# Performance work log

Measured on AMD Instinct MI355X. Metric: run time of the kernel, lower is better.

Reference implementation:

```python
import jax, jax.numpy as jnp
import numpy as np

HEADS = 8
DIM_HEAD = 64
DIM = 512
SCALE = DIM ** -0.5  # NOTE: original scales by dim**-0.5, not dim_head**-0.5


def setup_inputs() -> dict:
    key = jax.random.key(0)
    k1, k2, k3 = jax.random.split(key, 3)
    b, n = 2, 4096
    x = jax.random.normal(k1, (b, n, DIM), dtype=jnp.float32)
    Wqkv = jax.random.normal(k2, (DIM, 3 * HEADS * DIM_HEAD), dtype=jnp.float32) * (DIM ** -0.5)
    Wout = jax.random.normal(k3, (HEADS * DIM_HEAD, DIM), dtype=jnp.float32) * ((HEADS * DIM_HEAD) ** -0.5)
    b_out = jnp.zeros((DIM,), dtype=jnp.float32)
    return {"x": x, "Wqkv": Wqkv, "Wout": Wout, "b_out": b_out}


def reference(x, Wqkv, Wout, b_out):
    b, n, _ = x.shape
    h, d = HEADS, DIM_HEAD
    qkv = x @ Wqkv  # [b, n, 3*h*d]
    q, k, v = jnp.split(qkv, 3, axis=-1)
    to_heads = lambda t: t.reshape(b, n, h, d).transpose(0, 2, 1, 3)  # [b,h,n,d]
    q, k, v = to_heads(q), to_heads(k), to_heads(v)
    half = n // 2
    q_s, q_t = q[:, :, :half], q[:, :, half:]
    k_t = k[:, :, half:]  # k_s is unused in the original module
    v_s, v_t = v[:, :, :half], v[:, :, half:]
    # temporal branch: q_t attends to k_t, reads v_t
    dots_t = jnp.einsum('bhid,bhjd->bhij', q_t, k_t) * SCALE
    # spatial branch: cross-term q_s attends to k_t, reads v_s
    dots_s = jnp.einsum('bhid,bhjd->bhij', q_s, k_t) * SCALE
    attn_s = jax.nn.softmax(dots_s, axis=-1)
    attn_t = jax.nn.softmax(dots_t, axis=-1)
    out_s = jnp.einsum('bhij,bhjd->bhid', attn_s, v_s)
    out_t = jnp.einsum('bhij,bhjd->bhid', attn_t, v_t)
    out = jnp.concatenate([out_s, out_t], axis=2)  # [b,h,n,d]
    out = out.transpose(0, 2, 1, 3).reshape(b, n, h * d)
    return out @ Wout + b_out
```

## Files before the change

### kernel.cpp

```cpp
#include <hip/hip_runtime.h>
#include <hip/hip_bf16.h>

typedef __bf16 bf16;
typedef _Float16 f16;
typedef __bf16 bf16x4 __attribute__((ext_vector_type(4)));
typedef __bf16 bf16x8 __attribute__((ext_vector_type(8)));
typedef _Float16 f16x4 __attribute__((ext_vector_type(4)));
typedef _Float16 f16x8 __attribute__((ext_vector_type(8)));
typedef float floatx4 __attribute__((ext_vector_type(4)));

static __device__ __forceinline__ floatx4 mfma_bf16(bf16x8 a, bf16x8 b, floatx4 c) {
  return __builtin_amdgcn_mfma_f32_16x16x32_bf16(a, b, c, 0, 0, 0);
}
static __device__ __forceinline__ floatx4 mfma_f16k16(f16x4 a, f16x4 b, floatx4 c) {
  return __builtin_amdgcn_mfma_f32_16x16x16f16(a, b, c, 0, 0, 0);
}

static __device__ __forceinline__ bf16x8 ldcvt8(const float* __restrict__ src) {
  float4 f0 = *reinterpret_cast<const float4*>(src);
  float4 f1 = *reinterpret_cast<const float4*>(src + 4);
  bf16x8 r;
  r[0] = (bf16)f0.x; r[1] = (bf16)f0.y; r[2] = (bf16)f0.z; r[3] = (bf16)f0.w;
  r[4] = (bf16)f1.x; r[5] = (bf16)f1.y; r[6] = (bf16)f1.z; r[7] = (bf16)f1.w;
  return r;
}

#define HEADS 8
#define DIMH 64
#define DIM 512
#define SEQ 4096
#define HALF 2048
#define BATCH 2
#define MROWS (BATCH * SEQ)
#define ELEMS ((size_t)MROWS * DIM)

#define C2F (0.044194173824159216f * 1.4426950408889634f)

__global__ __launch_bounds__(256)
void transpose_cvt(const float* __restrict__ src, bf16* __restrict__ dst,
                   int K, int N) {
  __shared__ float tile[32][33];
  const int n0 = blockIdx.x * 32, k0 = blockIdx.y * 32;
  const int t = threadIdx.x;
  const int r = t >> 3, c4 = (t & 7) * 4;
  float4 v = *reinterpret_cast<const float4*>(src + (size_t)(k0 + r) * N + n0 + c4);
  tile[r][c4 + 0] = v.x; tile[r][c4 + 1] = v.y;
  tile[r][c4 + 2] = v.z; tile[r][c4 + 3] = v.w;
  __syncthreads();
  bf16x4 o;
#pragma unroll
  for (int i = 0; i < 4; ++i) o[i] = (bf16)tile[c4 + i][r];
  *reinterpret_cast<bf16x4*>(dst + (size_t)(n0 + r) * K + k0 + c4) = o;
}

__global__ __launch_bounds__(256)
void qkv_gemm(const float* __restrict__ X, const bf16* __restrict__ Wt,
              bf16* __restrict__ Qw, bf16* __restrict__ Kw, f16* __restrict__ Vt) {
  constexpr int Kd = DIM;
  __shared__ __align__(16) bf16 smem[5120];
  bf16 (*As)[40] = (bf16(*)[40])smem;
  bf16 (*Bs)[40] = (bf16(*)[40])(smem + 2560);
  f16 (*Ts)[72] = (f16(*)[72])smem;

  const int m0 = blockIdx.x * 64, n0 = blockIdx.y * 64;
  const int t = threadIdx.x;
  const int wave = t >> 6, lane = t & 63, quad = lane >> 4, l16 = lane & 15;
  const int m_off = (wave >> 1) * 32, n_off = (wave & 1) * 32;

  floatx4 acc[2][2] = {};
  const int srow = t >> 2, scol = (t & 3) * 8;

  for (int k0 = 0; k0 < Kd; k0 += 32) {
    bf16x8 av = ldcvt8(X + (size_t)(m0 + srow) * Kd + k0 + scol);
    bf16x8 bv = *reinterpret_cast<const bf16x8*>(Wt + (size_t)(n0 + srow) * Kd + k0 + scol);
    *reinterpret_cast<bf16x8*>(&As[srow][scol]) = av;
    *reinterpret_cast<bf16x8*>(&Bs[srow][scol]) = bv;
    __syncthreads();

    bf16x8 a0 = *reinterpret_cast<const bf16x8*>(&As[m_off + l16][quad * 8]);
    bf16x8 a1 = *reinterpret_cast<const bf16x8*>(&As[m_off + 16 + l16][quad * 8]);
    bf16x8 b0 = *reinterpret_cast<const bf16x8*>(&Bs[n_off + l16][quad * 8]);
    bf16x8 b1 = *reinterpret_cast<const bf16x8*>(&Bs[n_off + 16 + l16][quad * 8]);
    acc[0][0] = mfma_bf16(a0, b0, acc[0][0]);
    acc[0][1] = mfma_bf16(a0, b1, acc[0][1]);
    acc[1][0] = mfma_bf16(a1, b0, acc[1][0]);
    acc[1][1] = mfma_bf16(a1, b1, acc[1][1]);
    __syncthreads();
  }

  if (n0 < 1024) {
#pragma unroll
    for (int mi = 0; mi < 2; ++mi)
#pragma unroll
      for (int ni = 0; ni < 2; ++ni)
#pragma unroll
        for (int r = 0; r < 4; ++r) {
          int row = m0 + m_off + mi * 16 + quad * 4 + r;
          int col = n0 + n_off + ni * 16 + l16;
          int which = col >> 9, cc = col & 511;
          int head = cc >> 6, dim = cc & 63;
          int bb = row >> 12, nn = row & 4095;
          float val = acc[mi][ni][r];
          if (which == 0) val *= C2F;
          bf16* dst = which ? Kw : Qw;
          dst[(((size_t)(bb * HEADS + head)) * SEQ + nn) * DIMH + dim] = (bf16)val;
        }
  } else {
    int head = (n0 - 1024) >> 6;
#pragma unroll
    for (int mi = 0; mi < 2; ++mi)
#pragma unroll
      for (int ni = 0; ni < 2; ++ni)
#pragma unroll
        for (int r = 0; r < 4; ++r)
          Ts[n_off + ni * 16 + l16][m_off + mi * 16 + quad * 4 + r] = (f16)acc[mi][ni][r];
    __syncthreads();
    int bb = m0 >> 12, nnb = m0 & 4095;
    size_t base = ((size_t)(bb * HEADS + head)) * DIMH;
#pragma unroll
    for (int it = 0; it < 2; ++it) {
      int idx = t + it * 256;
      int dim = idx >> 3, ns = (idx & 7) * 8;
      *reinterpret_cast<f16x8*>(Vt + (base + dim) * SEQ + nnb + ns) =
          *reinterpret_cast<const f16x8*>(&Ts[dim][ns]);
    }
  }
}

__global__ __launch_bounds__(256)
void attn_kernel(const bf16* __restrict__ Q, const bf16* __restrict__ K,
                 const f16* __restrict__ Vt, bf16* __restrict__ Ow) {
  const int qt = blockIdx.x, h = blockIdx.y, bb = blockIdx.z;
  const int t = threadIdx.x;
  const int wave = t >> 6, lane = t & 63, quad = lane >> 4, l16 = lane & 15;

  __shared__ bf16 Ks[64][72];
  __shared__ f16 VsT[64][72];

  const size_t hb = ((size_t)(bb * HEADS + h)) * SEQ * DIMH;
  const int vbase = (qt < 16) ? 0 : HALF;
  const int q0 = qt * 128 + wave * 32;

  bf16x8 qa[2][2];
#pragma unroll
  for (int mt = 0; mt < 2; ++mt)
#pragma unroll
    for (int kc = 0; kc < 2; ++kc)
      qa[mt][kc] = *reinterpret_cast<const bf16x8*>(
          Q + hb + (size_t)(q0 + mt * 16 + l16) * DIMH + kc * 32 + quad * 8);

  floatx4 o_acc[2][4] = {};
  float l_acc[2] = {0.f, 0.f};

  for (int kc0 = 0; kc0 < HALF; kc0 += 64) {
    __syncthreads();
#pragma unroll
    for (int it = 0; it < 2; ++it) {
      int idx = t + it * 256;
      int row = idx >> 3, g = idx & 7;
      bf16x8 kv = *reinterpret_cast<const bf16x8*>(
          K + hb + (size_t)(HALF + kc0 + row) * DIMH + g * 8);
      *reinterpret_cast<bf16x8*>(&Ks[row][g * 8]) = kv;
      f16x8 vv = *reinterpret_cast<const f16x8*>(
          Vt + hb + (size_t)row * SEQ + vbase + kc0 + g * 8);
      *reinterpret_cast<f16x8*>(&VsT[row][g * 8]) = vv;
    }
    __syncthreads();

#pragma unroll
    for (int kt = 0; kt < 4; ++kt) {
      bf16x8 ka0 = *reinterpret_cast<const bf16x8*>(&Ks[kt * 16 + l16][quad * 8]);
      bf16x8 ka1 = *reinterpret_cast<const bf16x8*>(&Ks[kt * 16 + l16][32 + quad * 8]);

      f16x4 pb[2];
#pragma unroll
      for (int mt = 0; mt < 2; ++mt) {
        floatx4 st = {0.f, 0.f, 0.f, 0.f};
        st = mfma_bf16(ka0, qa[mt][0], st);
        st = mfma_bf16(ka1, qa[mt][1], st);
        float lsum = l_acc[mt];
#pragma unroll
        for (int r = 0; r < 4; ++r) {
          float p = __builtin_amdgcn_exp2f(st[r]);
          lsum += p;
          pb[mt][r] = (f16)p;
        }
        l_acc[mt] = lsum;
      }

#pragma unroll
      for (int dsub = 0; dsub < 4; ++dsub) {
        f16x4 va = *reinterpret_cast<const f16x4*>(
            &VsT[dsub * 16 + l16][kt * 16 + quad * 4]);
        o_acc[0][dsub] = mfma_f16k16(va, pb[0], o_acc[0][dsub]);
        o_acc[1][dsub] = mfma_f16k16(va, pb[1], o_acc[1][dsub]);
      }
    }
  }

  float inv[2];
#pragma unroll
  for (int mt = 0; mt < 2; ++mt) {
    float v = l_acc[mt];
    v += __shfl_xor(v, 16);
    v += __shfl_xor(v, 32);
    inv[mt] = 1.0f / v;
  }

#pragma unroll
  for (int mt = 0; mt < 2; ++mt) {
    int n = q0 + mt * 16 + l16;
    size_t rowbase = ((size_t)(bb * SEQ + n)) * DIM + h * DIMH;
#pragma unroll
    for (int dsub = 0; dsub < 4; ++dsub) {
      bf16x4 ov;
#pragma unroll
      for (int r = 0; r < 4; ++r) ov[r] = (bf16)(o_acc[mt][dsub][r] * inv[mt]);
      *reinterpret_cast<bf16x4*>(Ow + rowbase + dsub * 16 + quad * 4) = ov;
    }
  }
}

__global__ __launch_bounds__(256)
void out_gemm(const bf16* __restrict__ A, const bf16* __restrict__ Wt,
              const float* __restrict__ bias, float* __restrict__ out) {
  constexpr int Kd = DIM;
  __shared__ bf16 As[64][40];
  __shared__ bf16 Bs[64][40];

  const int m0 = blockIdx.x * 64, n0 = blockIdx.y * 64;
  const int t = threadIdx.x;
  const int wave = t >> 6, lane = t & 63, quad = lane >> 4, l16 = lane & 15;
  const int m_off = (wave >> 1) * 32, n_off = (wave & 1) * 32;

  floatx4 acc[2][2] = {};
  const int srow = t >> 2, scol = (t & 3) * 8;

  for (int k0 = 0; k0 < Kd; k0 += 32) {
    bf16x8 av = *reinterpret_cast<const bf16x8*>(A + (size_t)(m0 + srow) * Kd + k0 + scol);
    bf16x8 bv = *reinterpret_cast<const bf16x8*>(Wt + (size_t)(n0 + srow) * Kd + k0 + scol);
    *reinterpret_cast<bf16x8*>(&As[srow][scol]) = av;
    *reinterpret_cast<bf16x8*>(&Bs[srow][scol]) = bv;
    __syncthreads();

    bf16x8 a0 = *reinterpret_cast<const bf16x8*>(&As[m_off + l16][quad * 8]);
    bf16x8 a1 = *reinterpret_cast<const bf16x8*>(&As[m_off + 16 + l16][quad * 8]);
    bf16x8 b0 = *reinterpret_cast<const bf16x8*>(&Bs[n_off + l16][quad * 8]);
    bf16x8 b1 = *reinterpret_cast<const bf16x8*>(&Bs[n_off + 16 + l16][quad * 8]);
    acc[0][0] = mfma_bf16(a0, b0, acc[0][0]);
    acc[0][1] = mfma_bf16(a0, b1, acc[0][1]);
    acc[1][0] = mfma_bf16(a1, b0, acc[1][0]);
    acc[1][1] = mfma_bf16(a1, b1, acc[1][1]);
    __syncthreads();
  }

#pragma unroll
  for (int mi = 0; mi < 2; ++mi)
#pragma unroll
    for (int ni = 0; ni < 2; ++ni)
#pragma unroll
      for (int r = 0; r < 4; ++r) {
        int row = m0 + m_off + mi * 16 + quad * 4 + r;
        int col = n0 + n_off + ni * 16 + l16;
        out[(size_t)row * DIM + col] = acc[mi][ni][r] + bias[col];
      }
}

extern "C" void kernel_launch(void* const* d_in, const int* in_sizes, int n_in,
                              void* d_out, int out_size, void* d_ws, size_t ws_size,
                              hipStream_t stream) {
  const float* x = (const float*)d_in[0];
  const float* wqkv = (const float*)d_in[1];
  const float* wout = (const float*)d_in[2];
  const float* bout = (const float*)d_in[3];
  float* out = (float*)d_out;

  bf16* Qw = (bf16*)d_ws;
  bf16* Kw = Qw + ELEMS;
  f16* Vt = (f16*)(Kw + ELEMS);
  bf16* Ow = (bf16*)(Vt + ELEMS);
  bf16* WtQKV = Ow + ELEMS;
  bf16* WtOUT = WtQKV + (size_t)1536 * 512;

  transpose_cvt<<<dim3(1536 / 32, DIM / 32), 256, 0, stream>>>(wqkv, WtQKV, DIM, 1536);
  transpose_cvt<<<dim3(DIM / 32, DIM / 32), 256, 0, stream>>>(wout, WtOUT, DIM, DIM);
  qkv_gemm<<<dim3(MROWS / 64, 1536 / 64), 256, 0, stream>>>(x, WtQKV, Qw, Kw, Vt);
  attn_kernel<<<dim3(SEQ / 128, HEADS, BATCH), 256, 0, stream>>>(Qw, Kw, Vt, Ow);
  out_gemm<<<dim3(MROWS / 64, DIM / 64), 256, 0, stream>>>(Ow, WtOUT, bout, out);
}
```

Baseline: 194.2 us.

## Retile QKV GEMM to 128x128, prefetch tiles in registers, shrink attention tiles

The QKV GEMM moves to 128x128 block tiles with 64x64 per wave and a register-prefetched next K slice, so each staged tile is reused more. The attention kernel handles 16 query rows per wave, 64 per block, which doubles the grid and adds register prefetch of K/V chunks plus an occupancy hint. The output GEMM also prefetches its next K slice into registers. The trade-off is more K/V reloads in attention and higher register pressure in the GEMM.

```diff
diff --git a/kernel.cpp b/kernel.cpp
--- a/kernel.cpp
+++ b/kernel.cpp
@@ -16,9 +16,7 @@
   return __builtin_amdgcn_mfma_f32_16x16x16f16(a, b, c, 0, 0, 0);
 }
 
-static __device__ __forceinline__ bf16x8 ldcvt8(const float* __restrict__ src) {
-  float4 f0 = *reinterpret_cast<const float4*>(src);
-  float4 f1 = *reinterpret_cast<const float4*>(src + 4);
+static __device__ __forceinline__ bf16x8 cvt8(float4 f0, float4 f1) {
   bf16x8 r;
   r[0] = (bf16)f0.x; r[1] = (bf16)f0.y; r[2] = (bf16)f0.z; r[3] = (bf16)f0.w;
   r[4] = (bf16)f1.x; r[5] = (bf16)f1.y; r[6] = (bf16)f1.z; r[7] = (bf16)f1.w;
@@ -56,47 +54,68 @@
 __global__ __launch_bounds__(256)
 void qkv_gemm(const float* __restrict__ X, const bf16* __restrict__ Wt,
               bf16* __restrict__ Qw, bf16* __restrict__ Kw, f16* __restrict__ Vt) {
-  constexpr int Kd = DIM;
-  __shared__ __align__(16) bf16 smem[5120];
-  bf16 (*As)[40] = (bf16(*)[40])smem;
-  bf16 (*Bs)[40] = (bf16(*)[40])(smem + 2560);
-  f16 (*Ts)[72] = (f16(*)[72])smem;
-
-  const int m0 = blockIdx.x * 64, n0 = blockIdx.y * 64;
+  __shared__ __align__(16) char smem_raw[36864];
+  bf16 (*As)[40] = (bf16(*)[40])smem_raw;
+  bf16 (*Bs)[40] = (bf16(*)[40])(smem_raw + 10240);
+
+  const int m0 = blockIdx.x * 128, n0 = blockIdx.y * 128;
   const int t = threadIdx.x;
   const int wave = t >> 6, lane = t & 63, quad = lane >> 4, l16 = lane & 15;
-  const int m_off = (wave >> 1) * 32, n_off = (wave & 1) * 32;
-
-  floatx4 acc[2][2] = {};
-  const int srow = t >> 2, scol = (t & 3) * 8;
-
-  for (int k0 = 0; k0 < Kd; k0 += 32) {
-    bf16x8 av = ldcvt8(X + (size_t)(m0 + srow) * Kd + k0 + scol);
-    bf16x8 bv = *reinterpret_cast<const bf16x8*>(Wt + (size_t)(n0 + srow) * Kd + k0 + scol);
-    *reinterpret_cast<bf16x8*>(&As[srow][scol]) = av;
-    *reinterpret_cast<bf16x8*>(&Bs[srow][scol]) = bv;
-    __syncthreads();
-
-    bf16x8 a0 = *reinterpret_cast<const bf16x8*>(&As[m_off + l16][quad * 8]);
-    bf16x8 a1 = *reinterpret_cast<const bf16x8*>(&As[m_off + 16 + l16][quad * 8]);
-    bf16x8 b0 = *reinterpret_cast<const bf16x8*>(&Bs[n_off + l16][quad * 8]);
-    bf16x8 b1 = *reinterpret_cast<const bf16x8*>(&Bs[n_off + 16 + l16][quad * 8]);
-    acc[0][0] = mfma_bf16(a0, b0, acc[0][0]);
-    acc[0][1] = mfma_bf16(a0, b1, acc[0][1]);
-    acc[1][0] = mfma_bf16(a1, b0, acc[1][0]);
-    acc[1][1] = mfma_bf16(a1, b1, acc[1][1]);
-    __syncthreads();
+  const int wr = wave >> 1, wc = wave & 1;
+
+  f16 (*Ts)[72] = (f16(*)[72])(smem_raw + wave * 9216);
+
+  floatx4 acc[4][4] = {};
+
+  float4 a0r[2], a1r[2];
+  bf16x8 breg[2];
+  auto loadk = [&](int k0) {
+#pragma unroll
+    for (int it = 0; it < 2; ++it) {
+      int idx = t + it * 256, row = idx >> 2, c8 = (idx & 3) * 8;
+      const float* xp = X + (size_t)(m0 + row) * DIM + k0 + c8;
+      a0r[it] = *reinterpret_cast<const float4*>(xp);
+      a1r[it] = *reinterpret_cast<const float4*>(xp + 4);
+      breg[it] = *reinterpret_cast<const bf16x8*>(Wt + (size_t)(n0 + row) * DIM + k0 + c8);
+    }
+  };
+
+  loadk(0);
+  for (int k0 = 0; k0 < DIM; k0 += 32) {
+    __syncthreads();
+#pragma unroll
+    for (int it = 0; it < 2; ++it) {
+      int idx = t + it * 256, row = idx >> 2, c8 = (idx & 3) * 8;
+      *reinterpret_cast<bf16x8*>(&As[row][c8]) = cvt8(a0r[it], a1r[it]);
+      *reinterpret_cast<bf16x8*>(&Bs[row][c8]) = breg[it];
+    }
+    __syncthreads();
+    int nk = k0 + 32; if (nk >= DIM) nk = 0;
+    loadk(nk);
+
+    bf16x8 af[4], bfr[4];
+#pragma unroll
+    for (int mi = 0; mi < 4; ++mi)
+      af[mi] = *reinterpret_cast<const bf16x8*>(&As[wr * 64 + mi * 16 + l16][quad * 8]);
+#pragma unroll
+    for (int ni = 0; ni < 4; ++ni)
+      bfr[ni] = *reinterpret_cast<const bf16x8*>(&Bs[wc * 64 + ni * 16 + l16][quad * 8]);
+#pragma unroll
+    for (int mi = 0; mi < 4; ++mi)
+#pragma unroll
+      for (int ni = 0; ni < 4; ++ni)
+        acc[mi][ni] = mfma_bf16(af[mi], bfr[ni], acc[mi][ni]);
   }
 
   if (n0 < 1024) {
 #pragma unroll
-    for (int mi = 0; mi < 2; ++mi)
-#pragma unroll
-      for (int ni = 0; ni < 2; ++ni)
+    for (int mi = 0; mi < 4; ++mi)
+#pragma unroll
+      for (int ni = 0; ni < 4; ++ni)
 #pragma unroll
         for (int r = 0; r < 4; ++r) {
-          int row = m0 + m_off + mi * 16 + quad * 4 + r;
-          int col = n0 + n_off + ni * 16 + l16;
+          int row = m0 + wr * 64 + mi * 16 + quad * 4 + r;
+          int col = n0 + wc * 64 + ni * 16 + l16;
           int which = col >> 9, cc = col & 511;
           int head = cc >> 6, dim = cc & 63;
           int bb = row >> 12, nn = row & 4095;
@@ -106,118 +125,115 @@
           dst[(((size_t)(bb * HEADS + head)) * SEQ + nn) * DIMH + dim] = (bf16)val;
         }
   } else {
-    int head = (n0 - 1024) >> 6;
-#pragma unroll
-    for (int mi = 0; mi < 2; ++mi)
-#pragma unroll
-      for (int ni = 0; ni < 2; ++ni)
-#pragma unroll
-        for (int r = 0; r < 4; ++r)
-          Ts[n_off + ni * 16 + l16][m_off + mi * 16 + quad * 4 + r] = (f16)acc[mi][ni][r];
-    __syncthreads();
-    int bb = m0 >> 12, nnb = m0 & 4095;
+    __syncthreads();
+    int head = (n0 + wc * 64 - 1024) >> 6;
+#pragma unroll
+    for (int mi = 0; mi < 4; ++mi)
+#pragma unroll
+      for (int ni = 0; ni < 4; ++ni) {
+        f16x4 pv;
+#pragma unroll
+        for (int r = 0; r < 4; ++r) pv[r] = (f16)acc[mi][ni][r];
+        *reinterpret_cast<f16x4*>(&Ts[ni * 16 + l16][mi * 16 + quad * 4]) = pv;
+      }
+    int bb = m0 >> 12, nnb = (m0 + wr * 64) & 4095;
     size_t base = ((size_t)(bb * HEADS + head)) * DIMH;
 #pragma unroll
-    for (int it = 0; it < 2; ++it) {
-      int idx = t + it * 256;
-      int dim = idx >> 3, ns = (idx & 7) * 8;
-      *reinterpret_cast<f16x8*>(Vt + (base + dim) * SEQ + nnb + ns) =
-          *reinterpret_cast<const f16x8*>(&Ts[dim][ns]);
-    }
-  }
-}
-
-__global__ __launch_bounds__(256)
+    for (int it = 0; it < 8; ++it) {
+      int idx = lane + it * 64;
+      int d = idx >> 3, ns = (idx & 7) * 8;
+      *reinterpret_cast<f16x8*>(Vt + (base + d) * SEQ + nnb + ns) =
+          *reinterpret_cast<const f16x8*>(&Ts[d][ns]);
+    }
+  }
+}
+
+__global__ __launch_bounds__(256, 4)
 void attn_kernel(const bf16* __restrict__ Q, const bf16* __restrict__ K,
                  const f16* __restrict__ Vt, bf16* __restrict__ Ow) {
   const int qt = blockIdx.x, h = blockIdx.y, bb = blockIdx.z;
   const int t = threadIdx.x;
-  const int wave = t >> 6, lane = t & 63, quad = lane >> 4, l16 = lane & 15;
+  const int lane = t & 63, quad = lane >> 4, l16 = lane & 15;
+  const int wave = t >> 6;
 
   __shared__ bf16 Ks[64][72];
   __shared__ f16 VsT[64][72];
 
   const size_t hb = ((size_t)(bb * HEADS + h)) * SEQ * DIMH;
-  const int vbase = (qt < 16) ? 0 : HALF;
-  const int q0 = qt * 128 + wave * 32;
-
-  bf16x8 qa[2][2];
-#pragma unroll
-  for (int mt = 0; mt < 2; ++mt)
-#pragma unroll
-    for (int kc = 0; kc < 2; ++kc)
-      qa[mt][kc] = *reinterpret_cast<const bf16x8*>(
-          Q + hb + (size_t)(q0 + mt * 16 + l16) * DIMH + kc * 32 + quad * 8);
-
-  floatx4 o_acc[2][4] = {};
-  float l_acc[2] = {0.f, 0.f};
-
+  const int vbase = (qt < 32) ? 0 : HALF;
+  const int q0 = qt * 64 + wave * 16;
+
+  bf16x8 qa[2];
+#pragma unroll
+  for (int kc = 0; kc < 2; ++kc)
+    qa[kc] = *reinterpret_cast<const bf16x8*>(
+        Q + hb + (size_t)(q0 + l16) * DIMH + kc * 32 + quad * 8);
+
+  floatx4 o_acc[4] = {};
+  float l_acc = 0.f;
+
+  bf16x8 kreg[2];
+  f16x8 vreg[2];
+  auto loadc = [&](int kc0) {
+#pragma unroll
+    for (int it = 0; it < 2; ++it) {
+      int idx = t + it * 256, row = idx >> 3, g8 = (idx & 7) * 8;
+      kreg[it] = *reinterpret_cast<const bf16x8*>(
+          K + hb + (size_t)(HALF + kc0 + row) * DIMH + g8);
+      vreg[it] = *reinterpret_cast<const f16x8*>(
+          Vt + hb + (size_t)row * SEQ + vbase + kc0 + g8);
+    }
+  };
+
+  loadc(0);
   for (int kc0 = 0; kc0 < HALF; kc0 += 64) {
     __syncthreads();
 #pragma unroll
     for (int it = 0; it < 2; ++it) {
-      int idx = t + it * 256;
-      int row = idx >> 3, g = idx & 7;
-      bf16x8 kv = *reinterpret_cast<const bf16x8*>(
-          K + hb + (size_t)(HALF + kc0 + row) * DIMH + g * 8);
-      *reinterpret_cast<bf16x8*>(&Ks[row][g * 8]) = kv;
-      f16x8 vv = *reinterpret_cast<const f16x8*>(
-          Vt + hb + (size_t)row * SEQ + vbase + kc0 + g * 8);
-      *reinterpret_cast<f16x8*>(&VsT[row][g * 8]) = vv;
-    }
-    __syncthreads();
+      int idx = t + it * 256, row = idx >> 3, g8 = (idx & 7) * 8;
+      *reinterpret_cast<bf16x8*>(&Ks[row][g8]) = kreg[it];
+      *reinterpret_cast<f16x8*>(&VsT[row][g8]) = vreg[it];
+    }
+    __syncthreads();
+    int nxt = kc0 + 64; if (nxt >= HALF) nxt = 0;
+    loadc(nxt);
 
 #pragma unroll
     for (int kt = 0; kt < 4; ++kt) {
       bf16x8 ka0 = *reinterpret_cast<const bf16x8*>(&Ks[kt * 16 + l16][quad * 8]);
       bf16x8 ka1 = *reinterpret_cast<const bf16x8*>(&Ks[kt * 16 + l16][32 + quad * 8]);
-
-      f16x4 pb[2];
-#pragma unroll
-      for (int mt = 0; mt < 2; ++mt) {
-        floatx4 st = {0.f, 0.f, 0.f, 0.f};
-        st = mfma_bf16(ka0, qa[mt][0], st);
-        st = mfma_bf16(ka1, qa[mt][1], st);
-        float lsum = l_acc[mt];
-#pragma unroll
-        for (int r = 0; r < 4; ++r) {
-          float p = __builtin_amdgcn_exp2f(st[r]);
-          lsum += p;
-          pb[mt][r] = (f16)p;
-        }
-        l_acc[mt] = lsum;
+      floatx4 st = {0.f, 0.f, 0.f, 0.f};
+      st = mfma_bf16(ka0, qa[0], st);
+      st = mfma_bf16(ka1, qa[1], st);
+      f16x4 pb;
+#pragma unroll
+      for (int r = 0; r < 4; ++r) {
+        float p = __builtin_amdgcn_exp2f(st[r]);
+        l_acc += p;
+        pb[r] = (f16)p;
       }
-
 #pragma unroll
       for (int dsub = 0; dsub < 4; ++dsub) {
         f16x4 va = *reinterpret_cast<const f16x4*>(
             &VsT[dsub * 16 + l16][kt * 16 + quad * 4]);
-        o_acc[0][dsub] = mfma_f16k16(va, pb[0], o_acc[0][dsub]);
-        o_acc[1][dsub] = mfma_f16k16(va, pb[1], o_acc[1][dsub]);
+        o_acc[dsub] = mfma_f16k16(va, pb, o_acc[dsub]);
       }
     }
   }
 
-  float inv[2];
-#pragma unroll
-  for (int mt = 0; mt < 2; ++mt) {
-    float v = l_acc[mt];
-    v += __shfl_xor(v, 16);
-    v += __shfl_xor(v, 32);
-    inv[mt] = 1.0f / v;
-  }
-
-#pragma unroll
-  for (int mt = 0; mt < 2; ++mt) {
-    int n = q0 + mt * 16 + l16;
-    size_t rowbase = ((size_t)(bb * SEQ + n)) * DIM + h * DIMH;
-#pragma unroll
-    for (int dsub = 0; dsub < 4; ++dsub) {
-      bf16x4 ov;
-#pragma unroll
-      for (int r = 0; r < 4; ++r) ov[r] = (bf16)(o_acc[mt][dsub][r] * inv[mt]);
-      *reinterpret_cast<bf16x4*>(Ow + rowbase + dsub * 16 + quad * 4) = ov;
-    }
+  float v = l_acc;
+  v += __shfl_xor(v, 16);
+  v += __shfl_xor(v, 32);
+  float inv = 1.0f / v;
+
+  int n = q0 + l16;
+  size_t rowbase = ((size_t)(bb * SEQ + n)) * DIM + h * DIMH;
+#pragma unroll
+  for (int dsub = 0; dsub < 4; ++dsub) {
+    bf16x4 ov;
+#pragma unroll
+    for (int r = 0; r < 4; ++r) ov[r] = (bf16)(o_acc[dsub][r] * inv);
+    *reinterpret_cast<bf16x4*>(Ow + rowbase + dsub * 16 + quad * 4) = ov;
   }
 }
 
@@ -236,12 +252,20 @@
   floatx4 acc[2][2] = {};
   const int srow = t >> 2, scol = (t & 3) * 8;
 
+  bf16x8 areg, breg;
+  auto loadk = [&](int k0) {
+    areg = *reinterpret_cast<const bf16x8*>(A + (size_t)(m0 + srow) * Kd + k0 + scol);
+    breg = *reinterpret_cast<const bf16x8*>(Wt + (size_t)(n0 + srow) * Kd + k0 + scol);
+  };
+
+  loadk(0);
   for (int k0 = 0; k0 < Kd; k0 += 32) {
-    bf16x8 av = *reinterpret_cast<const bf16x8*>(A + (size_t)(m0 + srow) * Kd + k0 + scol);
-    bf16x8 bv = *reinterpret_cast<const bf16x8*>(Wt + (size_t)(n0 + srow) * Kd + k0 + scol);
-    *reinterpret_cast<bf16x8*>(&As[srow][scol]) = av;
-    *reinterpret_cast<bf16x8*>(&Bs[srow][scol]) = bv;
-    __syncthreads();
+    __syncthreads();
+    *reinterpret_cast<bf16x8*>(&As[srow][scol]) = areg;
+    *reinterpret_cast<bf16x8*>(&Bs[srow][scol]) = breg;
+    __syncthreads();
+    int nk = k0 + 32; if (nk >= Kd) nk = 0;
+    loadk(nk);
 
     bf16x8 a0 = *reinterpret_cast<const bf16x8*>(&As[m_off + l16][quad * 8]);
     bf16x8 a1 = *reinterpret_cast<const bf16x8*>(&As[m_off + 16 + l16][quad * 8]);
@@ -251,7 +275,6 @@
     acc[0][1] = mfma_bf16(a0, b1, acc[0][1]);
     acc[1][0] = mfma_bf16(a1, b0, acc[1][0]);
     acc[1][1] = mfma_bf16(a1, b1, acc[1][1]);
-    __syncthreads();
   }
 
 #pragma unroll
@@ -284,7 +307,7 @@
 
   transpose_cvt<<<dim3(1536 / 32, DIM / 32), 256, 0, stream>>>(wqkv, WtQKV, DIM, 1536);
   transpose_cvt<<<dim3(DIM / 32, DIM / 32), 256, 0, stream>>>(wout, WtOUT, DIM, DIM);
-  qkv_gemm<<<dim3(MROWS / 64, 1536 / 64), 256, 0, stream>>>(x, WtQKV, Qw, Kw, Vt);
-  attn_kernel<<<dim3(SEQ / 128, HEADS, BATCH), 256, 0, stream>>>(Qw, Kw, Vt, Ow);
+  qkv_gemm<<<dim3(MROWS / 128, 1536 / 128), 256, 0, stream>>>(x, WtQKV, Qw, Kw, Vt);
+  attn_kernel<<<dim3(SEQ / 64, HEADS, BATCH), 256, 0, stream>>>(Qw, Kw, Vt, Ow);
   out_gemm<<<dim3(MROWS / 64, DIM / 64), 256, 0, stream>>>(Ow, WtOUT, bout, out);
 }
```

Measured after the change: 170.5 us. -12.2%, faster.
